# Performance work log

Measured on AMD Instinct MI355X. Metric: run time of the kernel, lower is better.

## Reference

```python
import jax, jax.numpy as jnp
import numpy as np

B, S, H, D, P = 16, 512, 12, 768, 256
TOP_RATE = 0.1
K = int(round(TOP_RATE * S))  # 51, matches round(self.top_rate * hidden_state.size(1))
LN_EPS = 1e-5


def setup_inputs() -> dict:
    key = jax.random.key(0)
    ks = jax.random.split(key, 6)
    return {
        "hidden_state": jax.random.normal(ks[0], (B, S, D), dtype=jnp.float32),
        "attention": jax.random.normal(ks[1], (B, H, S, S), dtype=jnp.float32),
        "length": S,  # uniform valid length (scalar int)
        # node_trans: Linear(D, P)
        "W_node": jax.random.normal(ks[2], (D, P), dtype=jnp.float32) * 0.02,
        "b_node": jnp.zeros((P,), dtype=jnp.float32),
        # node_eta parameter, initialized to 0 (self.node_eta.data.fill_(0))
        "node_eta": jnp.zeros((1,), dtype=jnp.float32),
        # fc: Linear(P, P)
        "W_fc": jax.random.normal(ks[3], (P, P), dtype=jnp.float32) * 0.02,
        "b_fc": jnp.zeros((P,), dtype=jnp.float32),
        # LayerNorm(P)
        "ln_gamma": jnp.ones((P,), dtype=jnp.float32),
        "ln_beta": jnp.zeros((P,), dtype=jnp.float32),
    }


def reference(hidden_state, attention, W_node, b_node, node_eta, W_fc, b_fc,
              ln_gamma, ln_beta, length):
    # average attention over heads: [B, S, S]
    avg_atten = attention.mean(axis=1)
    # per-target-node top-k neighbors
    vals, idx = jax.lax.top_k(avg_atten, K)  # [B, S, K]
    # edge mask replicating softmax(where(v>0, v, -1e9)) followed by nonzero():
    # entries at -1e9 underflow to exactly 0 in fp32 softmax iff the row has a
    # positive value; otherwise the softmax is uniform and all edges survive.
    keep = vals > 0.0
    row_has_pos = keep.any(axis=-1, keepdims=True)
    keep = jnp.where(row_has_pos, keep, True)            # [B, S, K] (>=1 True per row)
    keepf = keep.astype(hidden_state.dtype)[..., None]   # [B, S, K, 1]

    # node_trans on all nodes: [B, S, P]
    h = hidden_state @ W_node + b_node

    # gather source-node features h[b, idx[b, t, j], :] -> [B, S, K, P]
    gathered = jax.vmap(lambda hb, ib: hb[ib])(h, idx)

    # reduce='mean': edge weight w=1, mailbox mean over kept incoming edges
    h_agg = (gathered * keepf).sum(axis=2) / keepf.sum(axis=2)

    eta = node_eta[0]
    new_h = eta * h + (1.0 - eta) * h_agg                # [B, S, P]

    # dgl.mean_nodes: mean over the `length` nodes of each sub-graph (=S here)
    out = new_h.mean(axis=1)                             # [B, P]

    # fc(dropout(tanh(out))) with dropout in eval mode (identity)
    out = jnp.tanh(out) @ W_fc + b_fc

    # LayerNorm
    mu = out.mean(axis=-1, keepdims=True)
    var = ((out - mu) ** 2).mean(axis=-1, keepdims=True)
    out = (out - mu) / jnp.sqrt(var + LN_EPS) * ln_gamma + ln_beta
    return out
```

## Files before the change

### kernel.cpp

```cpp
#include <hip/hip_runtime.h>
#include <math.h>

#define B_ 16
#define S_ 512
#define H_ 12
#define D_ 768
#define P_ 256
#define K_ 51
#define CH_ 16
#define NCHUNK_ (S_/CH_)

__device__ __forceinline__ unsigned okey(float f) {
  unsigned u = __float_as_uint(f);
  return (u & 0x80000000u) ? ~u : (u | 0x80000000u);
}

__global__ __launch_bounds__(256) void k1_topk_mask(
    const float* __restrict__ attn, unsigned long long* __restrict__ maskbuf,
    float* __restrict__ invbuf) {
  const int tid = threadIdx.x;
  const int wv = tid >> 6;
  const int lane = tid & 63;
  const int bt = blockIdx.x * 4 + wv;
  const int b = bt >> 9;
  const int t = bt & (S_ - 1);

  const float* base = attn + (((size_t)b * H_) * S_ + t) * S_;
  float a[8] = {0.f, 0.f, 0.f, 0.f, 0.f, 0.f, 0.f, 0.f};
  #pragma unroll
  for (int h = 0; h < H_; ++h) {
    const float* r = base + (size_t)h * (S_ * S_);
    const float4 u = *(const float4*)(r + 4 * lane);
    const float4 v = *(const float4*)(r + 256 + 4 * lane);
    a[0] += u.x; a[1] += u.y; a[2] += u.z; a[3] += u.w;
    a[4] += v.x; a[5] += v.y; a[6] += v.z; a[7] += v.w;
  }
  unsigned k[8];
  #pragma unroll
  for (int i = 0; i < 8; ++i) {
    a[i] *= (1.0f / (float)H_);
    k[i] = okey(a[i]);
  }

  int p = 0;
  #pragma unroll
  for (int i = 0; i < 8; ++i) p += __popcll(__ballot(a[i] > 0.f));

  bool sel[8];
  float invcnt;
  if (p >= 1 && p < K_) {
    #pragma unroll
    for (int i = 0; i < 8; ++i) sel[i] = (a[i] > 0.f);
    invcnt = 1.0f / (float)p;
  } else {
    unsigned prefix = 0;
    int rem = K_;
    bool done = false;
    unsigned dmask = 0, thr = 0;
    for (int bpos = 31; bpos >= 0; --bpos) {
      const unsigned bit = 1u << bpos;
      const unsigned mb = ~(bit - 1u);
      const unsigned cand = prefix | bit;
      int cnt = 0;
      #pragma unroll
      for (int i = 0; i < 8; ++i)
        cnt += __popcll(__ballot((k[i] & mb) == cand));
      if (cnt == rem) { done = true; dmask = mb; thr = cand; break; }
      if (cnt > rem) prefix = cand;
      else rem -= cnt;
    }
    if (done) {
      #pragma unroll
      for (int i = 0; i < 8; ++i) sel[i] = (k[i] & dmask) >= thr;
    } else {
      const unsigned T = prefix;
      unsigned long long mm[8];
      #pragma unroll
      for (int i = 0; i < 8; ++i) mm[i] = __ballot(k[i] == T);
      const unsigned long long lt = ((unsigned long long)1 << lane) - 1ull;
      int fh = 0;
      #pragma unroll
      for (int i = 0; i < 4; ++i) fh += __popcll(mm[i]);
      #pragma unroll
      for (int i = 0; i < 8; ++i) {
        sel[i] = (k[i] > T);
        if (k[i] == T) {
          int r = 0;
          if (i < 4) {
            #pragma unroll
            for (int i2 = 0; i2 < 4; ++i2) r += __popcll(mm[i2] & lt);
            for (int i2 = 0; i2 < i; ++i2) r += (int)((mm[i2] >> lane) & 1ull);
          } else {
            r = fh;
            #pragma unroll
            for (int i2 = 4; i2 < 8; ++i2) r += __popcll(mm[i2] & lt);
            for (int i2 = 4; i2 < i; ++i2) r += (int)((mm[i2] >> lane) & 1ull);
          }
          if (r < rem) sel[i] = true;
        }
      }
    }
    invcnt = 1.0f / (float)K_;
  }

  unsigned long long m[8];
  #pragma unroll
  for (int i = 0; i < 8; ++i) m[i] = __ballot(sel[i]);
  if (lane == 0) {
    ulonglong2* mp = (ulonglong2*)(maskbuf + (size_t)bt * 8);
    mp[0] = ulonglong2{m[0], m[1]};
    mp[1] = ulonglong2{m[2], m[3]};
    mp[2] = ulonglong2{m[4], m[5]};
    mp[3] = ulonglong2{m[6], m[7]};
    invbuf[bt] = invcnt;
  }
}

__global__ __launch_bounds__(192) void k2_colsum_wsum(
    const unsigned long long* __restrict__ maskbuf,
    const float* __restrict__ invbuf, const float* __restrict__ node_eta,
    const float* __restrict__ hidden, float* __restrict__ x_part) {
  const int chunk = blockIdx.x;
  const int b = blockIdx.y;
  const int tid = threadIdx.x;
  __shared__ unsigned long long ld[S_ * 4];
  __shared__ float inv[S_];
  __shared__ float part[16][8];
  __shared__ float cs[CH_];

  const int wi0 = (chunk < 16) ? 0 : 4;
  for (int i = tid; i < S_ * 4; i += 192) {
    const int t = i >> 2, j = i & 3;
    ld[i] = maskbuf[(((size_t)b << 9) + t) * 8 + wi0 + j];
  }
  for (int i = tid; i < S_; i += 192) inv[i] = invbuf[(b << 9) + i];
  __syncthreads();

  if (tid < 128) {
    const int c = tid >> 3, g = tid & 7;
    const int s = chunk * CH_ + c;
    const int j = s & 3;
    const unsigned long long bm = 1ull << ((s & 255) >> 2);
    float w = 0.f;
    #pragma unroll 8
    for (int i = 0; i < 64; ++i) {
      const int t = i * 8 + g;
      if (ld[t * 4 + j] & bm) w += inv[t];
    }
    part[c][g] = w;
  }
  __syncthreads();
  if (tid < CH_) {
    float w = 0.f;
    #pragma unroll
    for (int g = 0; g < 8; ++g) w += part[tid][g];
    const float eta = node_eta[0];
    cs[tid] = (eta + (1.0f - eta) * w) * (1.0f / (float)S_);
  }
  __syncthreads();

  const float* hb = hidden + ((size_t)b * S_ + (size_t)chunk * CH_) * D_ + 4 * tid;
  float4 acc = make_float4(0.f, 0.f, 0.f, 0.f);
  #pragma unroll
  for (int s = 0; s < CH_; ++s) {
    const float4 v = *(const float4*)(hb + (size_t)s * D_);
    const float c = cs[s];
    acc.x += c * v.x; acc.y += c * v.y; acc.z += c * v.z; acc.w += c * v.w;
  }
  *(float4*)(x_part + ((size_t)chunk * B_ + b) * D_ + 4 * tid) = acc;
}

__global__ __launch_bounds__(256) void k3_tail(
    const float* __restrict__ x_part, const float* __restrict__ W_node,
    const float* __restrict__ b_node, const float* __restrict__ W_fc,
    const float* __restrict__ b_fc, const float* __restrict__ gamma,
    const float* __restrict__ beta, float* __restrict__ out) {
  const int b = blockIdx.x;
  const int tid = threadIdx.x;
  __shared__ float xs[D_];
  __shared__ float ts[P_];
  __shared__ float red[4];

  #pragma unroll
  for (int d = tid; d < D_; d += 256) {
    float s = 0.f;
    #pragma unroll 8
    for (int c = 0; c < NCHUNK_; ++c)
      s += x_part[((size_t)c * B_ + b) * D_ + d];
    xs[d] = s;
  }
  __syncthreads();

  float acc = 0.f;
  #pragma unroll 8
  for (int d = 0; d < D_; ++d) acc += xs[d] * W_node[(size_t)d * P_ + tid];
  ts[tid] = tanhf(acc + b_node[tid]);
  __syncthreads();

  float o = 0.f;
  #pragma unroll 8
  for (int q = 0; q < P_; ++q) o += ts[q] * W_fc[(size_t)q * P_ + tid];
  o += b_fc[tid];

  float s = o;
  #pragma unroll
  for (int off = 32; off > 0; off >>= 1) s += __shfl_down(s, off, 64);
  const int wave = tid >> 6, lane = tid & 63;
  if (lane == 0) red[wave] = s;
  __syncthreads();
  const float mu = (red[0] + red[1] + red[2] + red[3]) * (1.0f / (float)P_);
  __syncthreads();
  const float dv = o - mu;
  float s2 = dv * dv;
  #pragma unroll
  for (int off = 32; off > 0; off >>= 1) s2 += __shfl_down(s2, off, 64);
  if (lane == 0) red[wave] = s2;
  __syncthreads();
  const float var = (red[0] + red[1] + red[2] + red[3]) * (1.0f / (float)P_);
  const float inv = 1.0f / sqrtf(var + 1e-5f);
  out[b * P_ + tid] = dv * inv * gamma[tid] + beta[tid];
}

extern "C" void kernel_launch(void* const* d_in, const int* in_sizes, int n_in,
                              void* d_out, int out_size, void* d_ws, size_t ws_size,
                              hipStream_t stream) {
  (void)in_sizes; (void)n_in; (void)out_size; (void)ws_size;
  const float* hidden   = (const float*)d_in[0];
  const float* attn     = (const float*)d_in[1];
  const float* W_node   = (const float*)d_in[3];
  const float* b_node   = (const float*)d_in[4];
  const float* node_eta = (const float*)d_in[5];
  const float* W_fc     = (const float*)d_in[6];
  const float* b_fc     = (const float*)d_in[7];
  const float* gamma    = (const float*)d_in[8];
  const float* beta     = (const float*)d_in[9];
  float* out = (float*)d_out;

  unsigned long long* maskbuf = (unsigned long long*)d_ws;
  float* invbuf = (float*)(maskbuf + (size_t)B_ * S_ * 8);
  float* x_part = invbuf + B_ * S_;

  k1_topk_mask<<<(B_ * S_) / 4, 256, 0, stream>>>(attn, maskbuf, invbuf);
  k2_colsum_wsum<<<dim3(NCHUNK_, B_), 192, 0, stream>>>(maskbuf, invbuf,
                                                        node_eta, hidden, x_part);
  k3_tail<<<B_, 256, 0, stream>>>(x_part, W_node, b_node, W_fc, b_fc,
                                  gamma, beta, out);
}
```

Measured before the change: 382.9 us.

## Fuse three kernels into one cooperative persistent kernel with grid syncs

Merges the top-k mask, weighted column-sum and tail kernels into a single cooperative kernel of 512 blocks separated by grid-wide syncs. Each wave now processes four rows in a loop instead of one row per wave. The aim is to remove two kernel launch gaps. In exchange, the attention-streaming phase runs with fewer resident waves, which can reduce memory-level parallelism, and each grid sync adds a barrier cost.

```diff
diff --git a/kernel.cpp b/kernel.cpp
--- a/kernel.cpp
+++ b/kernel.cpp
@@ -1,5 +1,8 @@
 #include <hip/hip_runtime.h>
+#include <hip/hip_cooperative_groups.h>
 #include <math.h>
+
+namespace cg = cooperative_groups;
 
 #define B_ 16
 #define S_ 512
@@ -9,216 +12,236 @@
 #define K_ 51
 #define CH_ 16
 #define NCHUNK_ (S_/CH_)
+#define GRID_ 512
+#define RPW_ 4
 
 __device__ __forceinline__ unsigned okey(float f) {
   unsigned u = __float_as_uint(f);
   return (u & 0x80000000u) ? ~u : (u | 0x80000000u);
 }
 
-__global__ __launch_bounds__(256) void k1_topk_mask(
-    const float* __restrict__ attn, unsigned long long* __restrict__ maskbuf,
-    float* __restrict__ invbuf) {
+union SharedU {
+  struct {
+    unsigned long long ld[S_ * 4];
+    float inv[S_];
+    float part[16][8];
+    float cs[CH_];
+  } p2;
+  struct {
+    float xs[D_];
+    float ts[P_];
+    float red[4];
+  } p3;
+};
+
+__global__ __launch_bounds__(256) void fused_all(
+    const float* __restrict__ attn, const float* __restrict__ hidden,
+    const float* __restrict__ W_node, const float* __restrict__ b_node,
+    const float* __restrict__ node_eta, const float* __restrict__ W_fc,
+    const float* __restrict__ b_fc, const float* __restrict__ gamma,
+    const float* __restrict__ beta, float* __restrict__ out,
+    unsigned long long* __restrict__ maskbuf, float* __restrict__ invbuf,
+    float* __restrict__ x_part) {
+  __shared__ SharedU sh;
   const int tid = threadIdx.x;
   const int wv = tid >> 6;
   const int lane = tid & 63;
-  const int bt = blockIdx.x * 4 + wv;
-  const int b = bt >> 9;
-  const int t = bt & (S_ - 1);
-
-  const float* base = attn + (((size_t)b * H_) * S_ + t) * S_;
-  float a[8] = {0.f, 0.f, 0.f, 0.f, 0.f, 0.f, 0.f, 0.f};
-  #pragma unroll
-  for (int h = 0; h < H_; ++h) {
-    const float* r = base + (size_t)h * (S_ * S_);
-    const float4 u = *(const float4*)(r + 4 * lane);
-    const float4 v = *(const float4*)(r + 256 + 4 * lane);
-    a[0] += u.x; a[1] += u.y; a[2] += u.z; a[3] += u.w;
-    a[4] += v.x; a[5] += v.y; a[6] += v.z; a[7] += v.w;
+  const int wgid = blockIdx.x * 4 + wv;
+
+  #pragma unroll 1
+  for (int r = 0; r < RPW_; ++r) {
+    const int bt = wgid + 2048 * r;
+    const int b = bt >> 9;
+    const int t = bt & (S_ - 1);
+
+    const float* base = attn + (((size_t)b * H_) * S_ + t) * S_;
+    float a[8] = {0.f, 0.f, 0.f, 0.f, 0.f, 0.f, 0.f, 0.f};
+    #pragma unroll
+    for (int h = 0; h < H_; ++h) {
+      const float* rp = base + (size_t)h * (S_ * S_);
+      const float4 u = *(const float4*)(rp + 4 * lane);
+      const float4 v = *(const float4*)(rp + 256 + 4 * lane);
+      a[0] += u.x; a[1] += u.y; a[2] += u.z; a[3] += u.w;
+      a[4] += v.x; a[5] += v.y; a[6] += v.z; a[7] += v.w;
+    }
+    unsigned k[8];
+    #pragma unroll
+    for (int i = 0; i < 8; ++i) {
+      a[i] *= (1.0f / (float)H_);
+      k[i] = okey(a[i]);
+    }
+
+    int p = 0;
+    #pragma unroll
+    for (int i = 0; i < 8; ++i) p += __popcll(__ballot(a[i] > 0.f));
+
+    bool sel[8];
+    float invcnt;
+    if (p >= 1 && p < K_) {
+      #pragma unroll
+      for (int i = 0; i < 8; ++i) sel[i] = (a[i] > 0.f);
+      invcnt = 1.0f / (float)p;
+    } else {
+      unsigned prefix = 0;
+      int rem = K_;
+      bool done = false;
+      unsigned dmask = 0, thr = 0;
+      for (int bpos = 31; bpos >= 0; --bpos) {
+        const unsigned bit = 1u << bpos;
+        const unsigned mb = ~(bit - 1u);
+        const unsigned cand = prefix | bit;
+        int cnt = 0;
+        #pragma unroll
+        for (int i = 0; i < 8; ++i)
+          cnt += __popcll(__ballot((k[i] & mb) == cand));
+        if (cnt == rem) { done = true; dmask = mb; thr = cand; break; }
+        if (cnt > rem) prefix = cand;
+        else rem -= cnt;
+      }
+      if (done) {
+        #pragma unroll
+        for (int i = 0; i < 8; ++i) sel[i] = (k[i] & dmask) >= thr;
+      } else {
+        const unsigned T = prefix;
+        unsigned long long mm[8];
+        #pragma unroll
+        for (int i = 0; i < 8; ++i) mm[i] = __ballot(k[i] == T);
+        const unsigned long long lt = ((unsigned long long)1 << lane) - 1ull;
+        int fh = 0;
+        #pragma unroll
+        for (int i = 0; i < 4; ++i) fh += __popcll(mm[i]);
+        #pragma unroll
+        for (int i = 0; i < 8; ++i) {
+          sel[i] = (k[i] > T);
+          if (k[i] == T) {
+            int rr = 0;
+            if (i < 4) {
+              #pragma unroll
+              for (int i2 = 0; i2 < 4; ++i2) rr += __popcll(mm[i2] & lt);
+              for (int i2 = 0; i2 < i; ++i2) rr += (int)((mm[i2] >> lane) & 1ull);
+            } else {
+              rr = fh;
+              #pragma unroll
+              for (int i2 = 4; i2 < 8; ++i2) rr += __popcll(mm[i2] & lt);
+              for (int i2 = 4; i2 < i; ++i2) rr += (int)((mm[i2] >> lane) & 1ull);
+            }
+            if (rr < rem) sel[i] = true;
+          }
+        }
+      }
+      invcnt = 1.0f / (float)K_;
+    }
+
+    unsigned long long m[8];
+    #pragma unroll
+    for (int i = 0; i < 8; ++i) m[i] = __ballot(sel[i]);
+    if (lane == 0) {
+      ulonglong2* mp = (ulonglong2*)(maskbuf + (size_t)bt * 8);
+      mp[0] = ulonglong2{m[0], m[1]};
+      mp[1] = ulonglong2{m[2], m[3]};
+      mp[2] = ulonglong2{m[4], m[5]};
+      mp[3] = ulonglong2{m[6], m[7]};
+      invbuf[bt] = invcnt;
+    }
   }
-  unsigned k[8];
-  #pragma unroll
-  for (int i = 0; i < 8; ++i) {
-    a[i] *= (1.0f / (float)H_);
-    k[i] = okey(a[i]);
+
+  cg::this_grid().sync();
+
+  {
+    const int chunk = blockIdx.x & (NCHUNK_ - 1);
+    const int b = blockIdx.x >> 5;
+    const int wi0 = (chunk < 16) ? 0 : 4;
+    for (int i = tid; i < S_ * 4; i += 256) {
+      const int t = i >> 2, j = i & 3;
+      sh.p2.ld[i] = maskbuf[(((size_t)b << 9) + t) * 8 + wi0 + j];
+    }
+    for (int i = tid; i < S_; i += 256) sh.p2.inv[i] = invbuf[(b << 9) + i];
+    __syncthreads();
+
+    if (tid < 128) {
+      const int c = tid >> 3, g = tid & 7;
+      const int s = chunk * CH_ + c;
+      const int j = s & 3;
+      const unsigned long long bm = 1ull << ((s & 255) >> 2);
+      float w = 0.f;
+      #pragma unroll 8
+      for (int i = 0; i < 64; ++i) {
+        const int t = i * 8 + g;
+        if (sh.p2.ld[t * 4 + j] & bm) w += sh.p2.inv[t];
+      }
+      sh.p2.part[c][g] = w;
+    }
+    __syncthreads();
+    if (tid < CH_) {
+      float w = 0.f;
+      #pragma unroll
+      for (int g = 0; g < 8; ++g) w += sh.p2.part[tid][g];
+      const float eta = node_eta[0];
+      sh.p2.cs[tid] = (eta + (1.0f - eta) * w) * (1.0f / (float)S_);
+    }
+    __syncthreads();
+
+    if (tid < 192) {
+      const float* hb =
+          hidden + ((size_t)b * S_ + (size_t)chunk * CH_) * D_ + 4 * tid;
+      float4 acc = make_float4(0.f, 0.f, 0.f, 0.f);
+      #pragma unroll
+      for (int s = 0; s < CH_; ++s) {
+        const float4 v = *(const float4*)(hb + (size_t)s * D_);
+        const float c = sh.p2.cs[s];
+        acc.x += c * v.x; acc.y += c * v.y; acc.z += c * v.z; acc.w += c * v.w;
+      }
+      *(float4*)(x_part + ((size_t)chunk * B_ + b) * D_ + 4 * tid) = acc;
+    }
   }
 
-  int p = 0;
-  #pragma unroll
-  for (int i = 0; i < 8; ++i) p += __popcll(__ballot(a[i] > 0.f));
-
-  bool sel[8];
-  float invcnt;
-  if (p >= 1 && p < K_) {
-    #pragma unroll
-    for (int i = 0; i < 8; ++i) sel[i] = (a[i] > 0.f);
-    invcnt = 1.0f / (float)p;
-  } else {
-    unsigned prefix = 0;
-    int rem = K_;
-    bool done = false;
-    unsigned dmask = 0, thr = 0;
-    for (int bpos = 31; bpos >= 0; --bpos) {
-      const unsigned bit = 1u << bpos;
-      const unsigned mb = ~(bit - 1u);
-      const unsigned cand = prefix | bit;
-      int cnt = 0;
-      #pragma unroll
-      for (int i = 0; i < 8; ++i)
-        cnt += __popcll(__ballot((k[i] & mb) == cand));
-      if (cnt == rem) { done = true; dmask = mb; thr = cand; break; }
-      if (cnt > rem) prefix = cand;
-      else rem -= cnt;
-    }
-    if (done) {
-      #pragma unroll
-      for (int i = 0; i < 8; ++i) sel[i] = (k[i] & dmask) >= thr;
-    } else {
-      const unsigned T = prefix;
-      unsigned long long mm[8];
-      #pragma unroll
-      for (int i = 0; i < 8; ++i) mm[i] = __ballot(k[i] == T);
-      const unsigned long long lt = ((unsigned long long)1 << lane) - 1ull;
-      int fh = 0;
-      #pragma unroll
-      for (int i = 0; i < 4; ++i) fh += __popcll(mm[i]);
-      #pragma unroll
-      for (int i = 0; i < 8; ++i) {
-        sel[i] = (k[i] > T);
-        if (k[i] == T) {
-          int r = 0;
-          if (i < 4) {
-            #pragma unroll
-            for (int i2 = 0; i2 < 4; ++i2) r += __popcll(mm[i2] & lt);
-            for (int i2 = 0; i2 < i; ++i2) r += (int)((mm[i2] >> lane) & 1ull);
-          } else {
-            r = fh;
-            #pragma unroll
-            for (int i2 = 4; i2 < 8; ++i2) r += __popcll(mm[i2] & lt);
-            for (int i2 = 4; i2 < i; ++i2) r += (int)((mm[i2] >> lane) & 1ull);
-          }
-          if (r < rem) sel[i] = true;
-        }
-      }
-    }
-    invcnt = 1.0f / (float)K_;
+  cg::this_grid().sync();
+
+  if (blockIdx.x < B_) {
+    const int b = blockIdx.x;
+    #pragma unroll
+    for (int d = tid; d < D_; d += 256) {
+      float s = 0.f;
+      #pragma unroll 8
+      for (int c = 0; c < NCHUNK_; ++c)
+        s += x_part[((size_t)c * B_ + b) * D_ + d];
+      sh.p3.xs[d] = s;
+    }
+    __syncthreads();
+
+    float acc = 0.f;
+    #pragma unroll 8
+    for (int d = 0; d < D_; ++d) acc += sh.p3.xs[d] * W_node[(size_t)d * P_ + tid];
+    sh.p3.ts[tid] = tanhf(acc + b_node[tid]);
+    __syncthreads();
+
+    float o = 0.f;
+    #pragma unroll 8
+    for (int q = 0; q < P_; ++q) o += sh.p3.ts[q] * W_fc[(size_t)q * P_ + tid];
+    o += b_fc[tid];
+
+    float s = o;
+    #pragma unroll
+    for (int off = 32; off > 0; off >>= 1) s += __shfl_down(s, off, 64);
+    const int wave = tid >> 6, ln = tid & 63;
+    if (ln == 0) sh.p3.red[wave] = s;
+    __syncthreads();
+    const float mu =
+        (sh.p3.red[0] + sh.p3.red[1] + sh.p3.red[2] + sh.p3.red[3]) *
+        (1.0f / (float)P_);
+    __syncthreads();
+    const float dv = o - mu;
+    float s2 = dv * dv;
+    #pragma unroll
+    for (int off = 32; off > 0; off >>= 1) s2 += __shfl_down(s2, off, 64);
+    if (ln == 0) sh.p3.red[wave] = s2;
+    __syncthreads();
+    const float var =
+        (sh.p3.red[0] + sh.p3.red[1] + sh.p3.red[2] + sh.p3.red[3]) *
+        (1.0f / (float)P_);
+    const float inv = 1.0f / sqrtf(var + 1e-5f);
+    out[b * P_ + tid] = dv * inv * gamma[tid] + beta[tid];
   }
-
-  unsigned long long m[8];
-  #pragma unroll
-  for (int i = 0; i < 8; ++i) m[i] = __ballot(sel[i]);
-  if (lane == 0) {
-    ulonglong2* mp = (ulonglong2*)(maskbuf + (size_t)bt * 8);
-    mp[0] = ulonglong2{m[0], m[1]};
-    mp[1] = ulonglong2{m[2], m[3]};
-    mp[2] = ulonglong2{m[4], m[5]};
-    mp[3] = ulonglong2{m[6], m[7]};
-    invbuf[bt] = invcnt;
-  }
-}
-
-__global__ __launch_bounds__(192) void k2_colsum_wsum(
-    const unsigned long long* __restrict__ maskbuf,
-    const float* __restrict__ invbuf, const float* __restrict__ node_eta,
-    const float* __restrict__ hidden, float* __restrict__ x_part) {
-  const int chunk = blockIdx.x;
-  const int b = blockIdx.y;
-  const int tid = threadIdx.x;
-  __shared__ unsigned long long ld[S_ * 4];
-  __shared__ float inv[S_];
-  __shared__ float part[16][8];
-  __shared__ float cs[CH_];
-
-  const int wi0 = (chunk < 16) ? 0 : 4;
-  for (int i = tid; i < S_ * 4; i += 192) {
-    const int t = i >> 2, j = i & 3;
-    ld[i] = maskbuf[(((size_t)b << 9) + t) * 8 + wi0 + j];
-  }
-  for (int i = tid; i < S_; i += 192) inv[i] = invbuf[(b << 9) + i];
-  __syncthreads();
-
-  if (tid < 128) {
-    const int c = tid >> 3, g = tid & 7;
-    const int s = chunk * CH_ + c;
-    const int j = s & 3;
-    const unsigned long long bm = 1ull << ((s & 255) >> 2);
-    float w = 0.f;
-    #pragma unroll 8
-    for (int i = 0; i < 64; ++i) {
-      const int t = i * 8 + g;
-      if (ld[t * 4 + j] & bm) w += inv[t];
-    }
-    part[c][g] = w;
-  }
-  __syncthreads();
-  if (tid < CH_) {
-    float w = 0.f;
-    #pragma unroll
-    for (int g = 0; g < 8; ++g) w += part[tid][g];
-    const float eta = node_eta[0];
-    cs[tid] = (eta + (1.0f - eta) * w) * (1.0f / (float)S_);
-  }
-  __syncthreads();
-
-  const float* hb = hidden + ((size_t)b * S_ + (size_t)chunk * CH_) * D_ + 4 * tid;
-  float4 acc = make_float4(0.f, 0.f, 0.f, 0.f);
-  #pragma unroll
-  for (int s = 0; s < CH_; ++s) {
-    const float4 v = *(const float4*)(hb + (size_t)s * D_);
-    const float c = cs[s];
-    acc.x += c * v.x; acc.y += c * v.y; acc.z += c * v.z; acc.w += c * v.w;
-  }
-  *(float4*)(x_part + ((size_t)chunk * B_ + b) * D_ + 4 * tid) = acc;
-}
-
-__global__ __launch_bounds__(256) void k3_tail(
-    const float* __restrict__ x_part, const float* __restrict__ W_node,
-    const float* __restrict__ b_node, const float* __restrict__ W_fc,
-    const float* __restrict__ b_fc, const float* __restrict__ gamma,
-    const float* __restrict__ beta, float* __restrict__ out) {
-  const int b = blockIdx.x;
-  const int tid = threadIdx.x;
-  __shared__ float xs[D_];
-  __shared__ float ts[P_];
-  __shared__ float red[4];
-
-  #pragma unroll
-  for (int d = tid; d < D_; d += 256) {
-    float s = 0.f;
-    #pragma unroll 8
-    for (int c = 0; c < NCHUNK_; ++c)
-      s += x_part[((size_t)c * B_ + b) * D_ + d];
-    xs[d] = s;
-  }
-  __syncthreads();
-
-  float acc = 0.f;
-  #pragma unroll 8
-  for (int d = 0; d < D_; ++d) acc += xs[d] * W_node[(size_t)d * P_ + tid];
-  ts[tid] = tanhf(acc + b_node[tid]);
-  __syncthreads();
-
-  float o = 0.f;
-  #pragma unroll 8
-  for (int q = 0; q < P_; ++q) o += ts[q] * W_fc[(size_t)q * P_ + tid];
-  o += b_fc[tid];
-
-  float s = o;
-  #pragma unroll
-  for (int off = 32; off > 0; off >>= 1) s += __shfl_down(s, off, 64);
-  const int wave = tid >> 6, lane = tid & 63;
-  if (lane == 0) red[wave] = s;
-  __syncthreads();
-  const float mu = (red[0] + red[1] + red[2] + red[3]) * (1.0f / (float)P_);
-  __syncthreads();
-  const float dv = o - mu;
-  float s2 = dv * dv;
-  #pragma unroll
-  for (int off = 32; off > 0; off >>= 1) s2 += __shfl_down(s2, off, 64);
-  if (lane == 0) red[wave] = s2;
-  __syncthreads();
-  const float var = (red[0] + red[1] + red[2] + red[3]) * (1.0f / (float)P_);
-  const float inv = 1.0f / sqrtf(var + 1e-5f);
-  out[b * P_ + tid] = dv * inv * gamma[tid] + beta[tid];
 }
 
 extern "C" void kernel_launch(void* const* d_in, const int* in_sizes, int n_in,
@@ -240,9 +263,11 @@
   float* invbuf = (float*)(maskbuf + (size_t)B_ * S_ * 8);
   float* x_part = invbuf + B_ * S_;
 
-  k1_topk_mask<<<(B_ * S_) / 4, 256, 0, stream>>>(attn, maskbuf, invbuf);
-  k2_colsum_wsum<<<dim3(NCHUNK_, B_), 192, 0, stream>>>(maskbuf, invbuf,
-                                                        node_eta, hidden, x_part);
-  k3_tail<<<B_, 256, 0, stream>>>(x_part, W_node, b_node, W_fc, b_fc,
-                                  gamma, beta, out);
+  void* args[] = {
+      (void*)&attn, (void*)&hidden, (void*)&W_node, (void*)&b_node,
+      (void*)&node_eta, (void*)&W_fc, (void*)&b_fc, (void*)&gamma,
+      (void*)&beta, (void*)&out, (void*)&maskbuf, (void*)&invbuf,
+      (void*)&x_part};
+  hipLaunchCooperativeKernel((const void*)fused_all, dim3(GRID_), dim3(256),
+                             args, 0, stream);
 }
```

Result: slower. 513.1 us (+34.0%).
